# Kernel tuning notes

Measured on AMD Instinct MI355X. Metric: run time of the kernel, lower is better.

The kernel has to match this reference:

```python
import jax, jax.numpy as jnp
import numpy as np


def setup_inputs() -> dict:
    key = jax.random.key(0)
    k1, k2 = jax.random.split(key)
    B, Lq, Ls, D = 16, 2048, 2048, 512
    query = jax.random.normal(k1, (B, Lq, D), dtype=jnp.float32)
    support = jax.random.normal(k2, (B, Ls, D), dtype=jnp.float32)
    return {"query": query, "support": support}


def reference(query, support):
    # attn: [B, Lq, Ls] = softmax(query @ support^T, axis=-1)
    logits = jnp.einsum("bqd,bsd->bqs", query, support)
    attn = jax.nn.softmax(logits, axis=-1)
    # attended support: [B, Lq, D]
    attended = jnp.einsum("bqs,bsd->bqd", attn, support)
    # score: [B, Lq] = sum over D of query * attended
    score = jnp.sum(query * attended, axis=-1)
    return score
```

## Files before the change

### kernel.cpp

```cpp
#include <hip/hip_runtime.h>
#include <hip/hip_bf16.h>

#define B_  16
#define LQ  2048
#define LS  2048
#define DD  512
#define BQ  256
#define BS  256
#define BK  64
#define HK  32
#define NSB (LS / BS)
#define NKC (DD / BK)
#define NSPLIT 4

static_assert(NKC == 8, "stage>>3 math assumes NKC==8");

typedef short bf16x8 __attribute__((ext_vector_type(8)));
typedef float f32x4  __attribute__((ext_vector_type(4)));

__device__ __forceinline__ void load_lds16(const void* g, void* l) {
  __builtin_amdgcn_global_load_lds((const __attribute__((address_space(1))) void*)g,
                                   (__attribute__((address_space(3))) void*)l,
                                   16, 0, 0);
}

__device__ __forceinline__ unsigned short f2bf(float f) {
  union { float f; unsigned int u; } v; v.f = f;
  unsigned int r = v.u + 0x7fffu + ((v.u >> 16) & 1u);
  return (unsigned short)(r >> 16);
}

__global__ __launch_bounds__(256) void cvt_kernel(const float* __restrict__ Q,
                                                  const float* __restrict__ S,
                                                  unsigned short* __restrict__ Qw,
                                                  unsigned short* __restrict__ Sw) {
  const int half = gridDim.x >> 1;
  int blk = blockIdx.x;
  const float* src; unsigned short* dst;
  if (blk < half) { src = Q; dst = Qw; } else { src = S; dst = Sw; blk -= half; }
  const size_t n4 = (size_t)B_ * LQ * DD / 4;
  const size_t stride = (size_t)half * 256;
  for (size_t i = (size_t)blk * 256 + threadIdx.x; i < n4; i += stride) {
    float4 f = ((const float4*)src)[i];
    ushort4 u;
    u.x = f2bf(f.x); u.y = f2bf(f.y); u.z = f2bf(f.z); u.w = f2bf(f.w);
    ((ushort4*)dst)[i] = u;
  }
}

__global__ __launch_bounds__(512, 2) void attn_kernel(const unsigned short* __restrict__ Qw,
                                                      const unsigned short* __restrict__ Sw,
                                                      float* __restrict__ out,
                                                      float* __restrict__ pm,
                                                      float* __restrict__ pse,
                                                      float* __restrict__ psel,
                                                      int nsplit) {
  __shared__ __align__(16) unsigned short sQh[4][BQ * HK];
  __shared__ __align__(16) unsigned short sSh[4][BS * HK];

  const int pid = blockIdx.x + (blockIdx.y << 3) + (blockIdx.z << 7);
  const int nch = (nsplit << 7) >> 3;
  const int lid = (pid & 7) * nch + (pid >> 3);
  const int qb   = lid & 7;
  const int rest = lid >> 3;
  const int spl  = rest & (nsplit - 1);
  const int b    = rest >> (nsplit == 4 ? 2 : 0);

  const int tid  = threadIdx.x;
  const int w    = tid >> 6;
  const int lane = tid & 63;
  const int h    = w & 1;
  const int g    = w >> 1;
  const int col  = lane & 15;
  const int quad = lane >> 4;

  const int q0 = qb * BQ;
  const unsigned short* Qb = Qw + (size_t)b * LQ * DD;
  const unsigned short* Sb = Sw + (size_t)b * LS * DD;

  float mst[4] = { -INFINITY, -INFINITY, -INFINITY, -INFINITY };
  float se[4]  = { 0.f, 0.f, 0.f, 0.f };
  float sel[4] = { 0.f, 0.f, 0.f, 0.f };

  f32x4 acc[8][4];
#pragma unroll
  for (int st = 0; st < 8; ++st)
#pragma unroll
    for (int qt = 0; qt < 4; ++qt)
      acc[st][qt] = (f32x4){0.f, 0.f, 0.f, 0.f};

  const int cc8 = (((lane & 3) ^ ((lane >> 3) & 3)) * 8);
  const int rl  = lane >> 2;
  const int koq = ((quad ^ ((col >> 1) & 3)) * 8);

  const int sbs = spl * (NSB / nsplit);
  const int nst = (NSB / nsplit) * NKC;
  const int U   = nst * 2;

  auto issue_half = [&](int u) {
    const int t  = u >> 1;
    const int k0 = (t & 7) * 64 + (u & 1) * 32;
    const int slot = u & 3;
    if (w < 4) {
      const unsigned short* gp = Qb + (size_t)(q0 + w * 64 + rl) * DD + k0 + cc8;
      unsigned short* lp = &sQh[slot][(w * 64) * HK];
#pragma unroll
      for (int i = 0; i < 4; ++i)
        load_lds16(gp + (size_t)i * 16 * DD, lp + i * 16 * HK);
    } else {
      const int sb = sbs + (t >> 3);
      const unsigned short* gp = Sb + (size_t)(sb * BS + (w - 4) * 64 + rl) * DD + k0 + cc8;
      unsigned short* lp = &sSh[slot][((w - 4) * 64) * HK];
#pragma unroll
      for (int i = 0; i < 4; ++i)
        load_lds16(gp + (size_t)i * 16 * DD, lp + i * 16 * HK);
    }
  };

  issue_half(0); issue_half(1); issue_half(2);

#pragma unroll 1
  for (int u = 0; u < U; ++u) {
    if (u < U - 2)       asm volatile("s_waitcnt vmcnt(8)" ::: "memory");
    else if (u == U - 2) asm volatile("s_waitcnt vmcnt(4)" ::: "memory");
    else                 asm volatile("s_waitcnt vmcnt(0)" ::: "memory");
    __builtin_amdgcn_s_barrier();
    if (u + 3 < U) issue_half(u + 3);

    const unsigned short* bq = &sQh[u & 3][0];
    const unsigned short* bs = &sSh[u & 3][0];

    bf16x8 aq[4], asv[4];
#pragma unroll
    for (int qt = 0; qt < 4; ++qt)
      aq[qt] = *(const bf16x8*)&bq[(g * 64 + qt * 16 + col) * HK + koq];
#pragma unroll
    for (int st = 0; st < 4; ++st)
      asv[st] = *(const bf16x8*)&bs[(h * 128 + st * 16 + col) * HK + koq];
    asm volatile("s_waitcnt lgkmcnt(0)" ::: "memory");
    __builtin_amdgcn_sched_barrier(0);
    __builtin_amdgcn_s_setprio(1);
#pragma unroll
    for (int qt = 0; qt < 4; ++qt)
#pragma unroll
      for (int st = 0; st < 4; ++st)
        acc[st][qt] = __builtin_amdgcn_mfma_f32_16x16x32_bf16(asv[st], aq[qt], acc[st][qt], 0, 0, 0);
    __builtin_amdgcn_s_setprio(0);

#pragma unroll
    for (int st = 0; st < 4; ++st)
      asv[st] = *(const bf16x8*)&bs[(h * 128 + (4 + st) * 16 + col) * HK + koq];
    asm volatile("s_waitcnt lgkmcnt(0)" ::: "memory");
    __builtin_amdgcn_sched_barrier(0);
    __builtin_amdgcn_s_setprio(1);
#pragma unroll
    for (int qt = 0; qt < 4; ++qt)
#pragma unroll
      for (int st = 0; st < 4; ++st)
        acc[4 + st][qt] = __builtin_amdgcn_mfma_f32_16x16x32_bf16(asv[st], aq[qt], acc[4 + st][qt], 0, 0, 0);
    __builtin_amdgcn_s_setprio(0);

    if ((u & (2 * NKC - 1)) == 2 * NKC - 1) {
#pragma unroll
      for (int qt = 0; qt < 4; ++qt) {
        float lmax = mst[qt];
#pragma unroll
        for (int st = 0; st < 8; ++st)
#pragma unroll
          for (int r = 0; r < 4; ++r)
            lmax = fmaxf(lmax, acc[st][qt][r]);
        lmax = fmaxf(lmax, __shfl_xor(lmax, 16, 64));
        lmax = fmaxf(lmax, __shfl_xor(lmax, 32, 64));
        float alpha = __expf(mst[qt] - lmax);
        float pe = 0.f, pel = 0.f;
#pragma unroll
        for (int st = 0; st < 8; ++st)
#pragma unroll
          for (int r = 0; r < 4; ++r) {
            float l = acc[st][qt][r];
            float e = __expf(l - lmax);
            pe += e;
            pel = fmaf(e, l, pel);
          }
        pe  += __shfl_xor(pe, 16, 64);  pe  += __shfl_xor(pe, 32, 64);
        pel += __shfl_xor(pel, 16, 64); pel += __shfl_xor(pel, 32, 64);
        se[qt]  = fmaf(se[qt],  alpha, pe);
        sel[qt] = fmaf(sel[qt], alpha, pel);
        mst[qt] = lmax;
#pragma unroll
        for (int st = 0; st < 8; ++st)
          acc[st][qt] = (f32x4){0.f, 0.f, 0.f, 0.f};
      }
    }
  }

  __syncthreads();
  float* red = (float*)&sQh[0][0];
  if (quad == 0) {
#pragma unroll
    for (int qt = 0; qt < 4; ++qt) {
      int qq = g * 64 + qt * 16 + col;
      red[h * 256 + qq]        = mst[qt];
      red[512 + h * 256 + qq]  = se[qt];
      red[1024 + h * 256 + qq] = sel[qt];
    }
  }
  __syncthreads();
  if (h == 0 && quad == 0) {
#pragma unroll
    for (int qt = 0; qt < 4; ++qt) {
      int qq = g * 64 + qt * 16 + col;
      float m0 = red[qq],       m1 = red[256 + qq];
      float M  = fmaxf(m0, m1);
      float a0 = __expf(m0 - M), a1 = __expf(m1 - M);
      float SE  = red[512 + qq]  * a0 + red[512 + 256 + qq]  * a1;
      float SEL = red[1024 + qq] * a0 + red[1024 + 256 + qq] * a1;
      size_t qi = (size_t)b * LQ + q0 + qq;
      if (nsplit == 1) {
        out[qi] = SEL / SE;
      } else {
        pm[qi * NSPLIT + spl]   = M;
        pse[qi * NSPLIT + spl]  = SE;
        psel[qi * NSPLIT + spl] = SEL;
      }
    }
  }
}

__global__ __launch_bounds__(256) void combine_kernel(const float* __restrict__ pm,
                                                      const float* __restrict__ pse,
                                                      const float* __restrict__ psel,
                                                      float* __restrict__ out) {
  int i = blockIdx.x * blockDim.x + threadIdx.x;
  if (i >= B_ * LQ) return;
  float M = -INFINITY;
#pragma unroll
  for (int s = 0; s < NSPLIT; ++s) M = fmaxf(M, pm[i * NSPLIT + s]);
  float SE = 0.f, SEL = 0.f;
#pragma unroll
  for (int s = 0; s < NSPLIT; ++s) {
    float a = __expf(pm[i * NSPLIT + s] - M);
    SE  = fmaf(pse[i * NSPLIT + s],  a, SE);
    SEL = fmaf(psel[i * NSPLIT + s], a, SEL);
  }
  out[i] = SEL / SE;
}

__global__ __launch_bounds__(256) void fallback_kernel(const float* __restrict__ Q,
                                                       const float* __restrict__ S,
                                                       float* __restrict__ out) {
  __shared__ float qv[DD];
  __shared__ float red[256];
  const int b = blockIdx.y, qi = blockIdx.x, tid = threadIdx.x;
  const float* qrow = Q + ((size_t)b * LQ + qi) * DD;
  for (int d = tid; d < DD; d += 256) qv[d] = qrow[d];
  __syncthreads();
  const float* Sb = S + (size_t)b * LS * DD;
  float m = -INFINITY, se = 0.f, sel = 0.f;
  for (int s = tid; s < LS; s += 256) {
    const float* srow = Sb + (size_t)s * DD;
    float dot = 0.f;
    for (int d = 0; d < DD; ++d) dot = fmaf(qv[d], srow[d], dot);
    float mn = fmaxf(m, dot);
    float a = __expf(m - mn);
    float e = __expf(dot - mn);
    se  = se * a + e;
    sel = sel * a + e * dot;
    m = mn;
  }
  red[tid] = m; __syncthreads();
  for (int o = 128; o > 0; o >>= 1) { if (tid < o) red[tid] = fmaxf(red[tid], red[tid + o]); __syncthreads(); }
  float M = red[0]; __syncthreads();
  float a = __expf(m - M); se *= a; sel *= a;
  red[tid] = se; __syncthreads();
  for (int o = 128; o > 0; o >>= 1) { if (tid < o) red[tid] += red[tid + o]; __syncthreads(); }
  float SE = red[0]; __syncthreads();
  red[tid] = sel; __syncthreads();
  for (int o = 128; o > 0; o >>= 1) { if (tid < o) red[tid] += red[tid + o]; __syncthreads(); }
  float SEL = red[0];
  if (tid == 0) out[(size_t)b * LQ + qi] = SEL / SE;
}

extern "C" void kernel_launch(void* const* d_in, const int* in_sizes, int n_in,
                              void* d_out, int out_size, void* d_ws, size_t ws_size,
                              hipStream_t stream) {
  const float* Q = (const float*)d_in[0];
  const float* S = (const float*)d_in[1];
  float* out = (float*)d_out;
  const size_t nelem = (size_t)B_ * LQ * DD;
  const size_t need_base  = 2 * nelem * sizeof(unsigned short);
  const size_t part_elems = (size_t)B_ * LQ * NSPLIT;
  const size_t need_split = need_base + 3 * part_elems * sizeof(float);

  if (ws_size >= need_base) {
    unsigned short* Qw = (unsigned short*)d_ws;
    unsigned short* Sw = Qw + nelem;
    cvt_kernel<<<2048, 256, 0, stream>>>(Q, S, Qw, Sw);
    if (ws_size >= need_split) {
      float* pm   = (float*)(Sw + nelem);
      float* pse  = pm + part_elems;
      float* psel = pse + part_elems;
      attn_kernel<<<dim3(LQ / BQ, B_, NSPLIT), 512, 0, stream>>>(Qw, Sw, out, pm, pse, psel, NSPLIT);
      combine_kernel<<<(B_ * LQ + 255) / 256, 256, 0, stream>>>(pm, pse, psel, out);
    } else {
      attn_kernel<<<dim3(LQ / BQ, B_, 1), 512, 0, stream>>>(Qw, Sw, out, nullptr, nullptr, nullptr, 1);
    }
  } else {
    fallback_kernel<<<dim3(LQ, B_), 256, 0, stream>>>(Q, S, out);
  }
}
```

Measured before the change: 220.8 us.

## Halve query tile to 128 rows with 256-thread blocks and triple-buffered LDS

Shrinks the query tile from 256 to 128 rows and the block from 512 to 256 threads, so the grid doubles and occupancy rises. All waves now load both Q and S slices, replacing the 4-slot buffer with a 3-slot ring prefetched two stages ahead. The prefetch is issued after the LDS fragment reads, and all S fragments are loaded up front so the second MFMA batch overlaps with the remaining LDS loads. Per-tile S reuse is halved, which increases global/L2 traffic for S in exchange for more blocks and better latency hiding.

```diff
diff --git a/kernel.cpp b/kernel.cpp
--- a/kernel.cpp
+++ b/kernel.cpp
@@ -5,7 +5,7 @@
 #define LQ  2048
 #define LS  2048
 #define DD  512
-#define BQ  256
+#define BQ  128
 #define BS  256
 #define BK  64
 #define HK  32
@@ -13,7 +13,7 @@
 #define NKC (DD / BK)
 #define NSPLIT 4
 
-static_assert(NKC == 8, "stage>>3 math assumes NKC==8");
+static_assert(NKC == 8, "stage math assumes NKC==8");
 
 typedef short bf16x8 __attribute__((ext_vector_type(8)));
 typedef float f32x4  __attribute__((ext_vector_type(4)));
@@ -48,21 +48,21 @@
   }
 }
 
-__global__ __launch_bounds__(512, 2) void attn_kernel(const unsigned short* __restrict__ Qw,
+__global__ __launch_bounds__(256, 2) void attn_kernel(const unsigned short* __restrict__ Qw,
                                                       const unsigned short* __restrict__ Sw,
                                                       float* __restrict__ out,
                                                       float* __restrict__ pm,
                                                       float* __restrict__ pse,
                                                       float* __restrict__ psel,
                                                       int nsplit) {
-  __shared__ __align__(16) unsigned short sQh[4][BQ * HK];
-  __shared__ __align__(16) unsigned short sSh[4][BS * HK];
-
-  const int pid = blockIdx.x + (blockIdx.y << 3) + (blockIdx.z << 7);
-  const int nch = (nsplit << 7) >> 3;
+  __shared__ __align__(16) unsigned short sQh[3][BQ * HK];
+  __shared__ __align__(16) unsigned short sSh[3][BS * HK];
+
+  const int pid = blockIdx.x + (blockIdx.y << 4) + (blockIdx.z << 8);
+  const int nch = (nsplit << 8) >> 3;
   const int lid = (pid & 7) * nch + (pid >> 3);
-  const int qb   = lid & 7;
-  const int rest = lid >> 3;
+  const int qb   = lid & 15;
+  const int rest = lid >> 4;
   const int spl  = rest & (nsplit - 1);
   const int b    = rest >> (nsplit == 4 ? 2 : 0);
 
@@ -97,46 +97,59 @@
   const int nst = (NSB / nsplit) * NKC;
   const int U   = nst * 2;
 
-  auto issue_half = [&](int u) {
+  auto issue_half = [&](int u, int slot) {
     const int t  = u >> 1;
     const int k0 = (t & 7) * 64 + (u & 1) * 32;
-    const int slot = u & 3;
-    if (w < 4) {
-      const unsigned short* gp = Qb + (size_t)(q0 + w * 64 + rl) * DD + k0 + cc8;
-      unsigned short* lp = &sQh[slot][(w * 64) * HK];
-#pragma unroll
-      for (int i = 0; i < 4; ++i)
-        load_lds16(gp + (size_t)i * 16 * DD, lp + i * 16 * HK);
-    } else {
-      const int sb = sbs + (t >> 3);
-      const unsigned short* gp = Sb + (size_t)(sb * BS + (w - 4) * 64 + rl) * DD + k0 + cc8;
-      unsigned short* lp = &sSh[slot][((w - 4) * 64) * HK];
-#pragma unroll
-      for (int i = 0; i < 4; ++i)
-        load_lds16(gp + (size_t)i * 16 * DD, lp + i * 16 * HK);
-    }
+    const int sb = sbs + (t >> 3);
+    const unsigned short* gq = Qb + (size_t)(q0 + w * 32 + rl) * DD + k0 + cc8;
+    unsigned short* lq = &sQh[slot][(w * 32) * HK];
+#pragma unroll
+    for (int i = 0; i < 2; ++i)
+      load_lds16(gq + (size_t)i * 16 * DD, lq + i * 16 * HK);
+    const unsigned short* gs = Sb + (size_t)(sb * BS + w * 64 + rl) * DD + k0 + cc8;
+    unsigned short* ls = &sSh[slot][(w * 64) * HK];
+#pragma unroll
+    for (int i = 0; i < 4; ++i)
+      load_lds16(gs + (size_t)i * 16 * DD, ls + i * 16 * HK);
   };
 
-  issue_half(0); issue_half(1); issue_half(2);
+  issue_half(0, 0);
+  issue_half(1, 1);
+  int cs = 0;
 
 #pragma unroll 1
   for (int u = 0; u < U; ++u) {
-    if (u < U - 2)       asm volatile("s_waitcnt vmcnt(8)" ::: "memory");
-    else if (u == U - 2) asm volatile("s_waitcnt vmcnt(4)" ::: "memory");
-    else                 asm volatile("s_waitcnt vmcnt(0)" ::: "memory");
+    if (u + 1 < U) asm volatile("s_waitcnt vmcnt(6)" ::: "memory");
+    else           asm volatile("s_waitcnt vmcnt(0)" ::: "memory");
     __builtin_amdgcn_s_barrier();
-    if (u + 3 < U) issue_half(u + 3);
-
-    const unsigned short* bq = &sQh[u & 3][0];
-    const unsigned short* bs = &sSh[u & 3][0];
-
-    bf16x8 aq[4], asv[4];
+
+    const unsigned short* bq = &sQh[cs][0];
+    const unsigned short* bs = &sSh[cs][0];
+
+    bf16x8 aq[4], as0[4], as1[4];
 #pragma unroll
     for (int qt = 0; qt < 4; ++qt)
       aq[qt] = *(const bf16x8*)&bq[(g * 64 + qt * 16 + col) * HK + koq];
 #pragma unroll
     for (int st = 0; st < 4; ++st)
-      asv[st] = *(const bf16x8*)&bs[(h * 128 + st * 16 + col) * HK + koq];
+      as0[st] = *(const bf16x8*)&bs[(h * 128 + st * 16 + col) * HK + koq];
+    __builtin_amdgcn_sched_barrier(0);
+#pragma unroll
+    for (int st = 0; st < 4; ++st)
+      as1[st] = *(const bf16x8*)&bs[(h * 128 + (4 + st) * 16 + col) * HK + koq];
+    {
+      int is = cs + 2; if (is >= 3) is -= 3;
+      if (u + 2 < U) issue_half(u + 2, is);
+    }
+    asm volatile("s_waitcnt lgkmcnt(4)" ::: "memory");
+    __builtin_amdgcn_sched_barrier(0);
+    __builtin_amdgcn_s_setprio(1);
+#pragma unroll
+    for (int qt = 0; qt < 4; ++qt)
+#pragma unroll
+      for (int st = 0; st < 4; ++st)
+        acc[st][qt] = __builtin_amdgcn_mfma_f32_16x16x32_bf16(as0[st], aq[qt], acc[st][qt], 0, 0, 0);
+    __builtin_amdgcn_s_setprio(0);
     asm volatile("s_waitcnt lgkmcnt(0)" ::: "memory");
     __builtin_amdgcn_sched_barrier(0);
     __builtin_amdgcn_s_setprio(1);
@@ -144,20 +157,7 @@
     for (int qt = 0; qt < 4; ++qt)
 #pragma unroll
       for (int st = 0; st < 4; ++st)
-        acc[st][qt] = __builtin_amdgcn_mfma_f32_16x16x32_bf16(asv[st], aq[qt], acc[st][qt], 0, 0, 0);
-    __builtin_amdgcn_s_setprio(0);
-
-#pragma unroll
-    for (int st = 0; st < 4; ++st)
-      asv[st] = *(const bf16x8*)&bs[(h * 128 + (4 + st) * 16 + col) * HK + koq];
-    asm volatile("s_waitcnt lgkmcnt(0)" ::: "memory");
-    __builtin_amdgcn_sched_barrier(0);
-    __builtin_amdgcn_s_setprio(1);
-#pragma unroll
-    for (int qt = 0; qt < 4; ++qt)
-#pragma unroll
-      for (int st = 0; st < 4; ++st)
-        acc[4 + st][qt] = __builtin_amdgcn_mfma_f32_16x16x32_bf16(asv[st], aq[qt], acc[4 + st][qt], 0, 0, 0);
+        acc[4 + st][qt] = __builtin_amdgcn_mfma_f32_16x16x32_bf16(as1[st], aq[qt], acc[4 + st][qt], 0, 0, 0);
     __builtin_amdgcn_s_setprio(0);
 
     if ((u & (2 * NKC - 1)) == 2 * NKC - 1) {
@@ -192,6 +192,7 @@
           acc[st][qt] = (f32x4){0.f, 0.f, 0.f, 0.f};
       }
     }
+    cs = (cs + 1 == 3) ? 0 : cs + 1;
   }
 
   __syncthreads();
@@ -200,9 +201,9 @@
 #pragma unroll
     for (int qt = 0; qt < 4; ++qt) {
       int qq = g * 64 + qt * 16 + col;
-      red[h * 256 + qq]        = mst[qt];
-      red[512 + h * 256 + qq]  = se[qt];
-      red[1024 + h * 256 + qq] = sel[qt];
+      red[h * 128 + qq]       = mst[qt];
+      red[256 + h * 128 + qq] = se[qt];
+      red[512 + h * 128 + qq] = sel[qt];
     }
   }
   __syncthreads();
@@ -210,11 +211,11 @@
 #pragma unroll
     for (int qt = 0; qt < 4; ++qt) {
       int qq = g * 64 + qt * 16 + col;
-      float m0 = red[qq],       m1 = red[256 + qq];
+      float m0 = red[qq],       m1 = red[128 + qq];
       float M  = fmaxf(m0, m1);
       float a0 = __expf(m0 - M), a1 = __expf(m1 - M);
-      float SE  = red[512 + qq]  * a0 + red[512 + 256 + qq]  * a1;
-      float SEL = red[1024 + qq] * a0 + red[1024 + 256 + qq] * a1;
+      float SE  = red[256 + qq] * a0 + red[256 + 128 + qq] * a1;
+      float SEL = red[512 + qq] * a0 + red[512 + 128 + qq] * a1;
       size_t qi = (size_t)b * LQ + q0 + qq;
       if (nsplit == 1) {
         out[qi] = SEL / SE;
@@ -300,10 +301,10 @@
       float* pm   = (float*)(Sw + nelem);
       float* pse  = pm + part_elems;
       float* psel = pse + part_elems;
-      attn_kernel<<<dim3(LQ / BQ, B_, NSPLIT), 512, 0, stream>>>(Qw, Sw, out, pm, pse, psel, NSPLIT);
+      attn_kernel<<<dim3(LQ / BQ, B_, NSPLIT), 256, 0, stream>>>(Qw, Sw, out, pm, pse, psel, NSPLIT);
       combine_kernel<<<(B_ * LQ + 255) / 256, 256, 0, stream>>>(pm, pse, psel, out);
     } else {
-      attn_kernel<<<dim3(LQ / BQ, B_, 1), 512, 0, stream>>>(Qw, Sw, out, nullptr, nullptr, nullptr, 1);
+      attn_kernel<<<dim3(LQ / BQ, B_, 1), 256, 0, stream>>>(Qw, Sw, out, nullptr, nullptr, nullptr, 1);
     }
   } else {
     fallback_kernel<<<dim3(LQ, B_), 256, 0, stream>>>(Q, S, out);
```

Result: no change. 222.2 us (+0.7%).
